# Kernel tuning notes

Hardware: AMD Instinct MI355X
Metric: run time of the kernel (lower is better)

Reference implementation:

```python
import jax, jax.numpy as jnp
import numpy as np

N_STATIONS = 35
N_PER_ST = 12
N_NODES = N_STATIONS * N_PER_ST   # 420
MAX_EDGES = 5120                  # true edge count = 34 * 12^2 = 4896
MAX_SUPER = 65536                 # true superedge candidates = 33*12*144 = 57024
PI = float(np.pi)

# constraint rows (r, phi, z) from the torch module
C_LO = jnp.array([269.0, -3.15, -2386.0], dtype=jnp.float32)
C_HI = jnp.array([581.0, 3.15, 2386.0], dtype=jnp.float32)


def _calc_dphi(p1, p2):
    d = p2 - p1
    d = jnp.where(d > PI, d - 2.0 * PI, d)
    return jnp.where(d < -PI, d + 2.0 * PI, d)


def _norm_node(v, k):
    return 2.0 * (v - C_LO[k]) / (C_HI[k] - C_LO[k]) - 1.0


def _norm_edge(v, k):
    return 2.0 * v / (C_HI[k] - C_LO[k])


def setup_inputs() -> dict:
    rng = np.random.default_rng(0)
    r = rng.uniform(270.0, 580.0, N_NODES)
    phi = rng.uniform(-3.1, 3.1, N_NODES)
    z = rng.uniform(-2000.0, 2000.0, N_NODES)
    station = np.arange(N_NODES) // N_PER_ST
    track = np.arange(N_NODES) % N_PER_ST  # one hit per track per station
    data = np.stack([
        np.zeros(N_NODES),          # event
        r * np.sin(phi),            # x (so atan2(x, y) = phi)
        r * np.cos(phi),            # y
        z,                          # z
        station.astype(np.float64),
        track.astype(np.float64),
        np.arange(N_NODES, dtype=np.float64),  # index_old
    ], axis=1).astype(np.float32)
    return {"event_data": jnp.asarray(data)}


def reference(event_data):
    x, y, z = event_data[:, 1], event_data[:, 2], event_data[:, 3]
    station, track, index_old = event_data[:, 4], event_data[:, 5], event_data[:, 6]
    # convert() : cartesian -> cylindrical (x<-r, y<-phi)
    r = jnp.sqrt(x * x + y * y)
    phi = jnp.arctan2(x, y)
    # get_graph(): adjacency of consecutive stations, row-major nonzero like torch
    adj = station[:, None] == (station[None, :] - 1.0)
    i_idx, j_idx = jnp.nonzero(adj, size=MAX_EDGES, fill_value=0)
    e_valid = jnp.arange(MAX_EDGES) < jnp.sum(adj)
    phi_p, phi_c = phi[i_idx], phi[j_idx]
    z_p, z_c = z[i_idx], z[j_idx]
    r_p, r_c = r[i_idx], r[j_idx]
    io_p, io_c = index_old[i_idx], index_old[j_idx]
    is_true = track[i_idx] == track[j_idx]  # torch leaves is_true uninitialized; defined as same-track
    dphi = _calc_dphi(phi_p, phi_c)
    dz, dx = z_c - z_p, r_c - r_p
    ez = (station[i_idx] + 1.0) / N_STATIONS
    e_index = jnp.arange(MAX_EDGES, dtype=event_data.dtype)
    # normalize() node-mode on endpoint phi/z (the only normalized cols used later) and edge-mode on dx,dy,dz
    yp_n, yc_n = _norm_node(phi_p, 1), _norm_node(phi_c, 1)
    zp_n, zc_n = _norm_node(z_p, 2), _norm_node(z_c, 2)
    dx_n, dy_n, dz_n = _norm_edge(dx, 0), _norm_edge(dphi, 1), _norm_edge(dz, 2)
    # apply_edge_restriction (masking instead of compaction)
    e_keep = e_valid & (dy_n > -10.0) & (dy_n < 10.0) & (dz_n > -10.0) & (dz_n < 10.0)
    # get_edges_from_supernodes: join first.index_old_c == second.index_old_p
    eq = (io_c[:, None] == io_p[None, :]) & e_keep[:, None] & e_keep[None, :]
    si, sj = jnp.nonzero(eq, size=MAX_SUPER, fill_value=0)
    s_valid = jnp.arange(MAX_SUPER) < jnp.sum(eq)
    d_first = jnp.stack([dx_n[si], dy_n[si], dz_n[si]], -1)
    d_second = jnp.stack([dx_n[sj], dy_n[sj], dz_n[sj]], -1)
    weight = jnp.linalg.norm(d_first - d_second, axis=1)
    # apply_weight_restriction: compact, order-preserving
    s_keep = s_valid & (weight < 0.1)
    (k_idx,) = jnp.nonzero(s_keep, size=MAX_SUPER, fill_value=0)
    k_valid = jnp.arange(MAX_SUPER) < jnp.sum(s_keep)
    fi, se = si[k_idx], sj[k_idx]
    su_is_true = is_true[fi] & is_true[se]
    su_ioc = jnp.where(k_valid, e_index[fi], -2.0)  # superedge index_old_c = first edge's index
    su_iop = jnp.where(k_valid, e_index[se], -2.0)  # superedge index_old_p = second edge's index
    su_y = jnp.where(k_valid, su_is_true.astype(event_data.dtype), 0.0)
    # construct_output_graph: nodes = (filtered) edges, edges = superedges
    node_idx = jnp.where(e_keep, e_index, -1.0)
    X = jnp.where(e_keep[:, None], jnp.stack([yp_n, yc_n, zp_n, zc_n, ez], -1), 0.0)
    Ri = node_idx[:, None] == su_ioc[None, :]   # [MAX_EDGES, MAX_SUPER] bool
    Ro = node_idx[:, None] == su_iop[None, :]
    super_ids = jnp.stack([su_iop, su_ioc], -1)
    edge_ids = jnp.where(e_keep[:, None], jnp.stack([io_p, io_c, e_index], -1), -1.0)
    return X, Ri, Ro, su_y, super_ids, node_idx, edge_ids
```

## Files before the change

kernel.cpp:

```cpp
#include <hip/hip_runtime.h>
#include <math.h>

#define NND 420
#define MAXE 5120
#define MAXS 65536

#define OFF_X    ((size_t)0)
#define OFF_RI   ((size_t)25600)
#define OFF_RO   ((size_t)(25600 + 335544320))
#define OFF_SUY  ((size_t)671114240)
#define OFF_SIDS ((size_t)671179776)
#define OFF_NIDX ((size_t)671310848)
#define OFF_EIDS ((size_t)671315968)

typedef float f4 __attribute__((ext_vector_type(4)));

static __device__ __forceinline__ float f32(double d) { return (float)d; }

__device__ float g_r[NND], g_phi[NND], g_z[NND], g_st[NND], g_trk[NND], g_io[NND];
__device__ short g_ei[MAXE], g_ej[MAXE];
__device__ int   g_estart[NND + 1];
__device__ float g_dxn[MAXE], g_dyn[MAXE], g_dzn[MAXE], g_iop[MAXE], g_ioc[MAXE];
__device__ int   g_keep[MAXE], g_istrue[MAXE], g_jn[MAXE];
__device__ int   g_cnt2[MAXE], g_off2[MAXE];
__device__ int   g_nedges, g_nkeep;

__global__ __launch_bounds__(256) void kFill(f4* __restrict__ p, size_t n4) {
    const size_t LO = OFF_SIDS >> 2;
    const size_t HI = (OFF_SIDS + 2 * (size_t)MAXS) >> 2;
    size_t i = (size_t)blockIdx.x * 256 + threadIdx.x;
    size_t stride = (size_t)gridDim.x * 256;
    const f4 z = {0.f, 0.f, 0.f, 0.f};
    const f4 m = {-2.f, -2.f, -2.f, -2.f};
    for (; i < n4; i += stride) {
        f4 v = (i >= LO && i < HI) ? m : z;
        __builtin_nontemporal_store(v, p + i);
    }
}

__global__ __launch_bounds__(512) void kA1(const float* __restrict__ ev) {
    __shared__ float s_st[NND];
    __shared__ int   s_scan[NND];
    int t = threadIdx.x;
    float stv = 0.0f;
    if (t < NND) {
        float x = ev[t * 7 + 1], y = ev[t * 7 + 2];
        g_r[t]   = sqrtf(__fadd_rn(__fmul_rn(x, x), __fmul_rn(y, y)));
        g_phi[t] = atan2f(x, y);
        g_z[t]   = ev[t * 7 + 3];
        stv      = ev[t * 7 + 4];
        g_st[t]  = stv;  s_st[t] = stv;
        g_trk[t] = ev[t * 7 + 5];
        g_io[t]  = ev[t * 7 + 6];
    }
    __syncthreads();
    int cnt = 0;
    if (t < NND) {
        float target = stv + 1.0f;
        for (int j = 0; j < NND; ++j) cnt += (s_st[j] == target) ? 1 : 0;
        s_scan[t] = cnt;
    }
    __syncthreads();
    for (int off = 1; off < NND; off <<= 1) {
        int v = 0;
        if (t < NND && t >= off) v = s_scan[t - off];
        __syncthreads();
        if (t < NND) s_scan[t] += v;
        __syncthreads();
    }
    if (t < NND) {
        int excl = s_scan[t] - cnt;
        g_estart[t] = excl > MAXE ? MAXE : excl;
        int k = excl;
        float target = stv + 1.0f;
        for (int j = 0; j < NND; ++j) {
            if (s_st[j] == target) {
                if (k < MAXE) { g_ei[k] = (short)t; g_ej[k] = (short)j; }
                ++k;
            }
        }
        if (t == NND - 1) {
            g_nedges = s_scan[t];
            g_estart[NND] = s_scan[t] > MAXE ? MAXE : s_scan[t];
        }
    }
}

__global__ __launch_bounds__(512) void kA2(float* __restrict__ out) {
    __shared__ float s_r[NND], s_phi[NND], s_z[NND], s_st[NND], s_trk[NND], s_io[NND];
    int t = threadIdx.x;
    for (int n = t; n < NND; n += 512) {
        s_r[n] = g_r[n]; s_phi[n] = g_phi[n]; s_z[n] = g_z[n];
        s_st[n] = g_st[n]; s_trk[n] = g_trk[n]; s_io[n] = g_io[n];
    }
    __syncthreads();

    const float PI_F  = f32(3.141592653589793);
    const float TPI_F = f32(6.283185307179586);
    const float LO1 = -3.15f, SPAN1 = 3.15f + 3.15f;
    const float LO2 = -2386.0f, SPAN2 = 4772.0f;
    const float SPAN0 = 312.0f;

    int k = blockIdx.x * 512 + t;
    if (k >= MAXE) return;
    int ne = g_nedges; if (ne > MAXE) ne = MAXE;
    bool valid = (k < ne);
    int i = valid ? (int)g_ei[k] : 0;
    int j = valid ? (int)g_ej[k] : 0;

    float phip = s_phi[i], phic = s_phi[j];
    float zp = s_z[i], zc = s_z[j];
    float rp = s_r[i], rc = s_r[j];
    float iop = s_io[i], ioc = s_io[j];
    int istrue = (s_trk[i] == s_trk[j]) ? 1 : 0;

    float d = __fsub_rn(phic, phip);
    if (d >  PI_F) d = __fsub_rn(d, TPI_F);
    if (d < -PI_F) d = __fadd_rn(d, TPI_F);

    float dzv = __fsub_rn(zc, zp);
    float dxv = __fsub_rn(rc, rp);
    float dxn = __fdiv_rn(__fmul_rn(2.0f, dxv), SPAN0);
    float dyn = __fdiv_rn(__fmul_rn(2.0f, d),   SPAN1);
    float dzn = __fdiv_rn(__fmul_rn(2.0f, dzv), SPAN2);

    bool keep = valid && (dyn > -10.0f) && (dyn < 10.0f)
                      && (dzn > -10.0f) && (dzn < 10.0f);

    float ypn = __fsub_rn(__fdiv_rn(__fmul_rn(2.0f, __fsub_rn(phip, LO1)), SPAN1), 1.0f);
    float ycn = __fsub_rn(__fdiv_rn(__fmul_rn(2.0f, __fsub_rn(phic, LO1)), SPAN1), 1.0f);
    float zpn = __fsub_rn(__fdiv_rn(__fmul_rn(2.0f, __fsub_rn(zp, LO2)), SPAN2), 1.0f);
    float zcn = __fsub_rn(__fdiv_rn(__fmul_rn(2.0f, __fsub_rn(zc, LO2)), SPAN2), 1.0f);
    float ez  = __fdiv_rn(__fadd_rn(s_st[i], 1.0f), 35.0f);

    size_t oX = OFF_X + (size_t)k * 5;
    out[oX + 0] = keep ? ypn : 0.0f;
    out[oX + 1] = keep ? ycn : 0.0f;
    out[oX + 2] = keep ? zpn : 0.0f;
    out[oX + 3] = keep ? zcn : 0.0f;
    out[oX + 4] = keep ? ez  : 0.0f;

    out[OFF_NIDX + (size_t)k] = keep ? (float)k : -1.0f;
    size_t oE = OFF_EIDS + (size_t)k * 3;
    out[oE + 0] = keep ? iop : -1.0f;
    out[oE + 1] = keep ? ioc : -1.0f;
    out[oE + 2] = keep ? (float)k : -1.0f;

    g_dxn[k] = dxn; g_dyn[k] = dyn; g_dzn[k] = dzn;
    g_iop[k] = iop; g_ioc[k] = ioc;
    g_keep[k] = keep ? 1 : 0; g_istrue[k] = istrue; g_jn[k] = j;
}

__global__ __launch_bounds__(256) void kB() {
    int gtid = blockIdx.x * 256 + threadIdx.x;
    int a = gtid >> 6, lane = gtid & 63;
    int c = 0;
    if (g_keep[a]) {
        int jn = g_jn[a];
        int b0 = g_estart[jn], b1 = g_estart[jn + 1];
        float ioca = g_ioc[a];
        float a0 = g_dxn[a], a1 = g_dyn[a], a2 = g_dzn[a];
        for (int b = b0 + lane; b < b1; b += 64) {
            if (g_keep[b] && (g_iop[b] == ioca)) {
                float d0 = __fsub_rn(a0, g_dxn[b]);
                float d1 = __fsub_rn(a1, g_dyn[b]);
                float d2 = __fsub_rn(a2, g_dzn[b]);
                float w = sqrtf(__fadd_rn(__fadd_rn(__fmul_rn(d0, d0),
                                                    __fmul_rn(d1, d1)),
                                          __fmul_rn(d2, d2)));
                if (w < 0.1f) ++c;
            }
        }
    }
    for (int off = 32; off; off >>= 1) c += __shfl_down(c, off, 64);
    if (lane == 0) g_cnt2[a] = c;
}

__global__ __launch_bounds__(1024) void kC() {
    __shared__ int part[1024];
    int t = threadIdx.x;
    int v[5]; int s = 0;
#pragma unroll
    for (int q = 0; q < 5; ++q) { v[q] = g_cnt2[t * 5 + q]; s += v[q]; }
    part[t] = s;
    __syncthreads();
    for (int off = 1; off < 1024; off <<= 1) {
        int x = (t >= off) ? part[t - off] : 0;
        __syncthreads();
        part[t] += x;
        __syncthreads();
    }
    int run = part[t] - s;
#pragma unroll
    for (int q = 0; q < 5; ++q) { g_off2[t * 5 + q] = run; run += v[q]; }
    if (t == 1023) g_nkeep = part[1023];
}

__global__ __launch_bounds__(256) void kD(float* __restrict__ out) {
    int gtid = blockIdx.x * 256 + threadIdx.x;
    int a = gtid >> 6, lane = gtid & 63;
    if (!g_keep[a]) return;
    int jn = g_jn[a];
    int b0 = g_estart[jn], b1 = g_estart[jn + 1];
    float ioca = g_ioc[a];
    float a0 = g_dxn[a], a1 = g_dyn[a], a2 = g_dzn[a];
    int ia = g_istrue[a];
    int base = g_off2[a];
    for (int cs = b0; cs < b1; cs += 64) {
        int b = cs + lane;
        bool pred = false;
        if (b < b1 && g_keep[b] && (g_iop[b] == ioca)) {
            float d0 = __fsub_rn(a0, g_dxn[b]);
            float d1 = __fsub_rn(a1, g_dyn[b]);
            float d2 = __fsub_rn(a2, g_dzn[b]);
            float w = sqrtf(__fadd_rn(__fadd_rn(__fmul_rn(d0, d0),
                                                __fmul_rn(d1, d1)),
                                      __fmul_rn(d2, d2)));
            pred = (w < 0.1f);
        }
        unsigned long long mask = __ballot(pred);
        if (pred) {
            int pos = base + (int)__popcll(mask & ((1ull << lane) - 1ull));
            if (pos < MAXS) {
                out[OFF_SUY + (size_t)pos] = (ia && g_istrue[b]) ? 1.0f : 0.0f;
                size_t os = OFF_SIDS + (size_t)pos * 2;
                out[os + 0] = (float)b;
                out[os + 1] = (float)a;
                out[OFF_RI + (size_t)a * MAXS + (size_t)pos] = 1.0f;
                out[OFF_RO + (size_t)b * MAXS + (size_t)pos] = 1.0f;
            }
        }
        base += (int)__popcll(mask);
    }
}

extern "C" void kernel_launch(void* const* d_in, const int* in_sizes, int n_in,
                              void* d_out, int out_size, void* d_ws, size_t ws_size,
                              hipStream_t stream) {
    const float* ev = (const float*)d_in[0];
    float* out = (float*)d_out;

    size_t n4 = (size_t)out_size / 4;
    hipLaunchKernelGGL(kFill, dim3(4096), dim3(256), 0, stream, (f4*)out, n4);
    hipLaunchKernelGGL(kA1, dim3(1), dim3(512), 0, stream, ev);
    hipLaunchKernelGGL(kA2, dim3((MAXE + 511) / 512), dim3(512), 0, stream, out);
    hipLaunchKernelGGL(kB, dim3(MAXE * 64 / 256), dim3(256), 0, stream);
    hipLaunchKernelGGL(kC, dim3(1), dim3(1024), 0, stream);
    hipLaunchKernelGGL(kD, dim3(MAXE * 64 / 256), dim3(256), 0, stream, out);
}
```

Measured before the change: 2.830 ms.

## Fuse edge, count, scan and scatter stages into one single-block kernel; use memset

```diff
diff --git a/kernel.cpp b/kernel.cpp
--- a/kernel.cpp
+++ b/kernel.cpp
@@ -17,83 +17,25 @@
 
 static __device__ __forceinline__ float f32(double d) { return (float)d; }
 
-__device__ float g_r[NND], g_phi[NND], g_z[NND], g_st[NND], g_trk[NND], g_io[NND];
-__device__ short g_ei[MAXE], g_ej[MAXE];
-__device__ int   g_estart[NND + 1];
 __device__ float g_dxn[MAXE], g_dyn[MAXE], g_dzn[MAXE], g_iop[MAXE], g_ioc[MAXE];
-__device__ int   g_keep[MAXE], g_istrue[MAXE], g_jn[MAXE];
-__device__ int   g_cnt2[MAXE], g_off2[MAXE];
-__device__ int   g_nedges, g_nkeep;
-
-__global__ __launch_bounds__(256) void kFill(f4* __restrict__ p, size_t n4) {
-    const size_t LO = OFF_SIDS >> 2;
-    const size_t HI = (OFF_SIDS + 2 * (size_t)MAXS) >> 2;
-    size_t i = (size_t)blockIdx.x * 256 + threadIdx.x;
-    size_t stride = (size_t)gridDim.x * 256;
-    const f4 z = {0.f, 0.f, 0.f, 0.f};
+__device__ int   g_keep[MAXE], g_istrue[MAXE];
+
+__global__ __launch_bounds__(256) void kSid(float* __restrict__ out) {
+    int i = blockIdx.x * 256 + threadIdx.x;
     const f4 m = {-2.f, -2.f, -2.f, -2.f};
-    for (; i < n4; i += stride) {
-        f4 v = (i >= LO && i < HI) ? m : z;
-        __builtin_nontemporal_store(v, p + i);
-    }
+    ((f4*)(out + OFF_SIDS))[i] = m;
 }
 
-__global__ __launch_bounds__(512) void kA1(const float* __restrict__ ev) {
-    __shared__ float s_st[NND];
-    __shared__ int   s_scan[NND];
-    int t = threadIdx.x;
-    float stv = 0.0f;
-    if (t < NND) {
-        float x = ev[t * 7 + 1], y = ev[t * 7 + 2];
-        g_r[t]   = sqrtf(__fadd_rn(__fmul_rn(x, x), __fmul_rn(y, y)));
-        g_phi[t] = atan2f(x, y);
-        g_z[t]   = ev[t * 7 + 3];
-        stv      = ev[t * 7 + 4];
-        g_st[t]  = stv;  s_st[t] = stv;
-        g_trk[t] = ev[t * 7 + 5];
-        g_io[t]  = ev[t * 7 + 6];
-    }
-    __syncthreads();
-    int cnt = 0;
-    if (t < NND) {
-        float target = stv + 1.0f;
-        for (int j = 0; j < NND; ++j) cnt += (s_st[j] == target) ? 1 : 0;
-        s_scan[t] = cnt;
-    }
-    __syncthreads();
-    for (int off = 1; off < NND; off <<= 1) {
-        int v = 0;
-        if (t < NND && t >= off) v = s_scan[t - off];
-        __syncthreads();
-        if (t < NND) s_scan[t] += v;
-        __syncthreads();
-    }
-    if (t < NND) {
-        int excl = s_scan[t] - cnt;
-        g_estart[t] = excl > MAXE ? MAXE : excl;
-        int k = excl;
-        float target = stv + 1.0f;
-        for (int j = 0; j < NND; ++j) {
-            if (s_st[j] == target) {
-                if (k < MAXE) { g_ei[k] = (short)t; g_ej[k] = (short)j; }
-                ++k;
-            }
-        }
-        if (t == NND - 1) {
-            g_nedges = s_scan[t];
-            g_estart[NND] = s_scan[t] > MAXE ? MAXE : s_scan[t];
-        }
-    }
-}
-
-__global__ __launch_bounds__(512) void kA2(float* __restrict__ out) {
+__global__ __launch_bounds__(1024) void kMono(const float* __restrict__ ev,
+                                              float* __restrict__ out) {
     __shared__ float s_r[NND], s_phi[NND], s_z[NND], s_st[NND], s_trk[NND], s_io[NND];
-    int t = threadIdx.x;
-    for (int n = t; n < NND; n += 512) {
-        s_r[n] = g_r[n]; s_phi[n] = g_phi[n]; s_z[n] = g_z[n];
-        s_st[n] = g_st[n]; s_trk[n] = g_trk[n]; s_io[n] = g_io[n];
-    }
-    __syncthreads();
+    __shared__ int   s_nscan[NND];
+    __shared__ int   s_estart[NND + 1];
+    __shared__ short s_ei[MAXE], s_ej[MAXE];
+    __shared__ int   s_cnt[MAXE];
+    __shared__ int   s_off2[MAXE];
+    __shared__ int   s_part[1024];
+    __shared__ int   s_ne;
 
     const float PI_F  = f32(3.141592653589793);
     const float TPI_F = f32(6.283185307179586);
@@ -101,136 +43,182 @@
     const float LO2 = -2386.0f, SPAN2 = 4772.0f;
     const float SPAN0 = 312.0f;
 
-    int k = blockIdx.x * 512 + t;
-    if (k >= MAXE) return;
-    int ne = g_nedges; if (ne > MAXE) ne = MAXE;
-    bool valid = (k < ne);
-    int i = valid ? (int)g_ei[k] : 0;
-    int j = valid ? (int)g_ej[k] : 0;
-
-    float phip = s_phi[i], phic = s_phi[j];
-    float zp = s_z[i], zc = s_z[j];
-    float rp = s_r[i], rc = s_r[j];
-    float iop = s_io[i], ioc = s_io[j];
-    int istrue = (s_trk[i] == s_trk[j]) ? 1 : 0;
-
-    float d = __fsub_rn(phic, phip);
-    if (d >  PI_F) d = __fsub_rn(d, TPI_F);
-    if (d < -PI_F) d = __fadd_rn(d, TPI_F);
-
-    float dzv = __fsub_rn(zc, zp);
-    float dxv = __fsub_rn(rc, rp);
-    float dxn = __fdiv_rn(__fmul_rn(2.0f, dxv), SPAN0);
-    float dyn = __fdiv_rn(__fmul_rn(2.0f, d),   SPAN1);
-    float dzn = __fdiv_rn(__fmul_rn(2.0f, dzv), SPAN2);
-
-    bool keep = valid && (dyn > -10.0f) && (dyn < 10.0f)
-                      && (dzn > -10.0f) && (dzn < 10.0f);
-
-    float ypn = __fsub_rn(__fdiv_rn(__fmul_rn(2.0f, __fsub_rn(phip, LO1)), SPAN1), 1.0f);
-    float ycn = __fsub_rn(__fdiv_rn(__fmul_rn(2.0f, __fsub_rn(phic, LO1)), SPAN1), 1.0f);
-    float zpn = __fsub_rn(__fdiv_rn(__fmul_rn(2.0f, __fsub_rn(zp, LO2)), SPAN2), 1.0f);
-    float zcn = __fsub_rn(__fdiv_rn(__fmul_rn(2.0f, __fsub_rn(zc, LO2)), SPAN2), 1.0f);
-    float ez  = __fdiv_rn(__fadd_rn(s_st[i], 1.0f), 35.0f);
-
-    size_t oX = OFF_X + (size_t)k * 5;
-    out[oX + 0] = keep ? ypn : 0.0f;
-    out[oX + 1] = keep ? ycn : 0.0f;
-    out[oX + 2] = keep ? zpn : 0.0f;
-    out[oX + 3] = keep ? zcn : 0.0f;
-    out[oX + 4] = keep ? ez  : 0.0f;
-
-    out[OFF_NIDX + (size_t)k] = keep ? (float)k : -1.0f;
-    size_t oE = OFF_EIDS + (size_t)k * 3;
-    out[oE + 0] = keep ? iop : -1.0f;
-    out[oE + 1] = keep ? ioc : -1.0f;
-    out[oE + 2] = keep ? (float)k : -1.0f;
-
-    g_dxn[k] = dxn; g_dyn[k] = dyn; g_dzn[k] = dzn;
-    g_iop[k] = iop; g_ioc[k] = ioc;
-    g_keep[k] = keep ? 1 : 0; g_istrue[k] = istrue; g_jn[k] = j;
-}
-
-__global__ __launch_bounds__(256) void kB() {
-    int gtid = blockIdx.x * 256 + threadIdx.x;
-    int a = gtid >> 6, lane = gtid & 63;
-    int c = 0;
-    if (g_keep[a]) {
-        int jn = g_jn[a];
-        int b0 = g_estart[jn], b1 = g_estart[jn + 1];
+    const int t = threadIdx.x;
+
+    float stv = 0.0f;
+    if (t < NND) {
+        float x = ev[t * 7 + 1], y = ev[t * 7 + 2];
+        s_r[t]   = sqrtf(__fadd_rn(__fmul_rn(x, x), __fmul_rn(y, y)));
+        s_phi[t] = atan2f(x, y);
+        s_z[t]   = ev[t * 7 + 3];
+        stv      = ev[t * 7 + 4];
+        s_st[t]  = stv;
+        s_trk[t] = ev[t * 7 + 5];
+        s_io[t]  = ev[t * 7 + 6];
+    }
+    __syncthreads();
+
+    int cnt = 0;
+    if (t < NND) {
+        float target = stv + 1.0f;
+        for (int j = 0; j < NND; ++j) cnt += (s_st[j] == target) ? 1 : 0;
+        s_nscan[t] = cnt;
+    }
+    __syncthreads();
+    for (int off = 1; off < NND; off <<= 1) {
+        int v = 0;
+        if (t < NND && t >= off) v = s_nscan[t - off];
+        __syncthreads();
+        if (t < NND) s_nscan[t] += v;
+        __syncthreads();
+    }
+    if (t < NND) {
+        int incl = s_nscan[t];
+        int excl = incl - cnt;
+        s_estart[t] = excl > MAXE ? MAXE : excl;
+        int k = excl;
+        float target = stv + 1.0f;
+        for (int j = 0; j < NND; ++j) {
+            if (s_st[j] == target) {
+                if (k < MAXE) { s_ei[k] = (short)t; s_ej[k] = (short)j; }
+                ++k;
+            }
+        }
+        if (t == NND - 1) {
+            int ne = incl > MAXE ? MAXE : incl;
+            s_ne = ne;
+            s_estart[NND] = ne;
+        }
+    }
+    __syncthreads();
+    const int ne = s_ne;
+
+    for (int k = t; k < MAXE; k += 1024) {
+        bool valid = (k < ne);
+        int i = valid ? (int)s_ei[k] : 0;
+        int j = valid ? (int)s_ej[k] : 0;
+
+        float phip = s_phi[i], phic = s_phi[j];
+        float zp = s_z[i], zc = s_z[j];
+        float rp = s_r[i], rc = s_r[j];
+        float iop = s_io[i], ioc = s_io[j];
+        int istrue = (s_trk[i] == s_trk[j]) ? 1 : 0;
+
+        float d = __fsub_rn(phic, phip);
+        if (d >  PI_F) d = __fsub_rn(d, TPI_F);
+        if (d < -PI_F) d = __fadd_rn(d, TPI_F);
+
+        float dzv = __fsub_rn(zc, zp);
+        float dxv = __fsub_rn(rc, rp);
+        float dxn = __fdiv_rn(__fmul_rn(2.0f, dxv), SPAN0);
+        float dyn = __fdiv_rn(__fmul_rn(2.0f, d),   SPAN1);
+        float dzn = __fdiv_rn(__fmul_rn(2.0f, dzv), SPAN2);
+
+        bool keep = valid && (dyn > -10.0f) && (dyn < 10.0f)
+                          && (dzn > -10.0f) && (dzn < 10.0f);
+
+        float ypn = __fsub_rn(__fdiv_rn(__fmul_rn(2.0f, __fsub_rn(phip, LO1)), SPAN1), 1.0f);
+        float ycn = __fsub_rn(__fdiv_rn(__fmul_rn(2.0f, __fsub_rn(phic, LO1)), SPAN1), 1.0f);
+        float zpn = __fsub_rn(__fdiv_rn(__fmul_rn(2.0f, __fsub_rn(zp, LO2)), SPAN2), 1.0f);
+        float zcn = __fsub_rn(__fdiv_rn(__fmul_rn(2.0f, __fsub_rn(zc, LO2)), SPAN2), 1.0f);
+        float ez  = __fdiv_rn(__fadd_rn(s_st[i], 1.0f), 35.0f);
+
+        size_t oX = OFF_X + (size_t)k * 5;
+        out[oX + 0] = keep ? ypn : 0.0f;
+        out[oX + 1] = keep ? ycn : 0.0f;
+        out[oX + 2] = keep ? zpn : 0.0f;
+        out[oX + 3] = keep ? zcn : 0.0f;
+        out[oX + 4] = keep ? ez  : 0.0f;
+
+        out[OFF_NIDX + (size_t)k] = keep ? (float)k : -1.0f;
+        size_t oE = OFF_EIDS + (size_t)k * 3;
+        out[oE + 0] = keep ? iop : -1.0f;
+        out[oE + 1] = keep ? ioc : -1.0f;
+        out[oE + 2] = keep ? (float)k : -1.0f;
+
+        g_dxn[k] = dxn; g_dyn[k] = dyn; g_dzn[k] = dzn;
+        g_iop[k] = iop; g_ioc[k] = ioc;
+        g_keep[k] = keep ? 1 : 0; g_istrue[k] = istrue;
+    }
+    __syncthreads();
+
+    const int w = t >> 6, lane = t & 63;
+    for (int a = w; a < MAXE; a += 16) {
+        int c = 0;
+        if (a < ne && g_keep[a]) {
+            int jn = (int)s_ej[a];
+            int b0 = s_estart[jn], b1 = s_estart[jn + 1];
+            float ioca = g_ioc[a];
+            float a0 = g_dxn[a], a1 = g_dyn[a], a2 = g_dzn[a];
+            for (int cs = b0; cs < b1; cs += 64) {
+                int b = cs + lane;
+                bool pred = false;
+                if (b < b1 && g_keep[b] && (g_iop[b] == ioca)) {
+                    float d0 = __fsub_rn(a0, g_dxn[b]);
+                    float d1 = __fsub_rn(a1, g_dyn[b]);
+                    float d2 = __fsub_rn(a2, g_dzn[b]);
+                    float wgt = sqrtf(__fadd_rn(__fadd_rn(__fmul_rn(d0, d0),
+                                                          __fmul_rn(d1, d1)),
+                                                __fmul_rn(d2, d2)));
+                    pred = (wgt < 0.1f);
+                }
+                c += (int)__popcll(__ballot(pred));
+            }
+        }
+        if (lane == 0) s_cnt[a] = c;
+    }
+    __syncthreads();
+
+    int v5[5]; int ssum = 0;
+#pragma unroll
+    for (int q = 0; q < 5; ++q) { v5[q] = s_cnt[t * 5 + q]; ssum += v5[q]; }
+    s_part[t] = ssum;
+    __syncthreads();
+    for (int off = 1; off < 1024; off <<= 1) {
+        int x = (t >= off) ? s_part[t - off] : 0;
+        __syncthreads();
+        s_part[t] += x;
+        __syncthreads();
+    }
+    int run = s_part[t] - ssum;
+#pragma unroll
+    for (int q = 0; q < 5; ++q) { s_off2[t * 5 + q] = run; run += v5[q]; }
+    __syncthreads();
+
+    for (int a = w; a < MAXE; a += 16) {
+        if (!(a < ne && g_keep[a])) continue;
+        int jn = (int)s_ej[a];
+        int b0 = s_estart[jn], b1 = s_estart[jn + 1];
         float ioca = g_ioc[a];
         float a0 = g_dxn[a], a1 = g_dyn[a], a2 = g_dzn[a];
-        for (int b = b0 + lane; b < b1; b += 64) {
-            if (g_keep[b] && (g_iop[b] == ioca)) {
+        int ia = g_istrue[a];
+        int base = s_off2[a];
+        for (int cs = b0; cs < b1; cs += 64) {
+            int b = cs + lane;
+            bool pred = false;
+            if (b < b1 && g_keep[b] && (g_iop[b] == ioca)) {
                 float d0 = __fsub_rn(a0, g_dxn[b]);
                 float d1 = __fsub_rn(a1, g_dyn[b]);
                 float d2 = __fsub_rn(a2, g_dzn[b]);
-                float w = sqrtf(__fadd_rn(__fadd_rn(__fmul_rn(d0, d0),
-                                                    __fmul_rn(d1, d1)),
-                                          __fmul_rn(d2, d2)));
-                if (w < 0.1f) ++c;
-            }
-        }
-    }
-    for (int off = 32; off; off >>= 1) c += __shfl_down(c, off, 64);
-    if (lane == 0) g_cnt2[a] = c;
-}
-
-__global__ __launch_bounds__(1024) void kC() {
-    __shared__ int part[1024];
-    int t = threadIdx.x;
-    int v[5]; int s = 0;
-#pragma unroll
-    for (int q = 0; q < 5; ++q) { v[q] = g_cnt2[t * 5 + q]; s += v[q]; }
-    part[t] = s;
-    __syncthreads();
-    for (int off = 1; off < 1024; off <<= 1) {
-        int x = (t >= off) ? part[t - off] : 0;
-        __syncthreads();
-        part[t] += x;
-        __syncthreads();
-    }
-    int run = part[t] - s;
-#pragma unroll
-    for (int q = 0; q < 5; ++q) { g_off2[t * 5 + q] = run; run += v[q]; }
-    if (t == 1023) g_nkeep = part[1023];
-}
-
-__global__ __launch_bounds__(256) void kD(float* __restrict__ out) {
-    int gtid = blockIdx.x * 256 + threadIdx.x;
-    int a = gtid >> 6, lane = gtid & 63;
-    if (!g_keep[a]) return;
-    int jn = g_jn[a];
-    int b0 = g_estart[jn], b1 = g_estart[jn + 1];
-    float ioca = g_ioc[a];
-    float a0 = g_dxn[a], a1 = g_dyn[a], a2 = g_dzn[a];
-    int ia = g_istrue[a];
-    int base = g_off2[a];
-    for (int cs = b0; cs < b1; cs += 64) {
-        int b = cs + lane;
-        bool pred = false;
-        if (b < b1 && g_keep[b] && (g_iop[b] == ioca)) {
-            float d0 = __fsub_rn(a0, g_dxn[b]);
-            float d1 = __fsub_rn(a1, g_dyn[b]);
-            float d2 = __fsub_rn(a2, g_dzn[b]);
-            float w = sqrtf(__fadd_rn(__fadd_rn(__fmul_rn(d0, d0),
-                                                __fmul_rn(d1, d1)),
-                                      __fmul_rn(d2, d2)));
-            pred = (w < 0.1f);
-        }
-        unsigned long long mask = __ballot(pred);
-        if (pred) {
-            int pos = base + (int)__popcll(mask & ((1ull << lane) - 1ull));
-            if (pos < MAXS) {
-                out[OFF_SUY + (size_t)pos] = (ia && g_istrue[b]) ? 1.0f : 0.0f;
-                size_t os = OFF_SIDS + (size_t)pos * 2;
-                out[os + 0] = (float)b;
-                out[os + 1] = (float)a;
-                out[OFF_RI + (size_t)a * MAXS + (size_t)pos] = 1.0f;
-                out[OFF_RO + (size_t)b * MAXS + (size_t)pos] = 1.0f;
-            }
-        }
-        base += (int)__popcll(mask);
+                float wgt = sqrtf(__fadd_rn(__fadd_rn(__fmul_rn(d0, d0),
+                                                      __fmul_rn(d1, d1)),
+                                            __fmul_rn(d2, d2)));
+                pred = (wgt < 0.1f);
+            }
+            unsigned long long mask = __ballot(pred);
+            if (pred) {
+                int pos = base + (int)__popcll(mask & ((1ull << lane) - 1ull));
+                if (pos < MAXS) {
+                    out[OFF_SUY + (size_t)pos] = (ia && g_istrue[b]) ? 1.0f : 0.0f;
+                    size_t os = OFF_SIDS + (size_t)pos * 2;
+                    out[os + 0] = (float)b;
+                    out[os + 1] = (float)a;
+                    out[OFF_RI + (size_t)a * MAXS + (size_t)pos] = 1.0f;
+                    out[OFF_RO + (size_t)b * MAXS + (size_t)pos] = 1.0f;
+                }
+            }
+            base += (int)__popcll(mask);
+        }
     }
 }
 
@@ -240,11 +228,7 @@
     const float* ev = (const float*)d_in[0];
     float* out = (float*)d_out;
 
-    size_t n4 = (size_t)out_size / 4;
-    hipLaunchKernelGGL(kFill, dim3(4096), dim3(256), 0, stream, (f4*)out, n4);
-    hipLaunchKernelGGL(kA1, dim3(1), dim3(512), 0, stream, ev);
-    hipLaunchKernelGGL(kA2, dim3((MAXE + 511) / 512), dim3(512), 0, stream, out);
-    hipLaunchKernelGGL(kB, dim3(MAXE * 64 / 256), dim3(256), 0, stream);
-    hipLaunchKernelGGL(kC, dim3(1), dim3(1024), 0, stream);
-    hipLaunchKernelGGL(kD, dim3(MAXE * 64 / 256), dim3(256), 0, stream, out);
+    hipMemsetAsync(d_out, 0, (size_t)out_size * sizeof(float), stream);
+    hipLaunchKernelGGL(kSid, dim3((MAXS * 2 / 4) / 256), dim3(256), 0, stream, out);
+    hipLaunchKernelGGL(kMono, dim3(1), dim3(1024), 0, stream, ev, out);
 }
```

After: 3.234 ms. +14.3%, slower.
